# Performance work log

Measured on AMD Instinct MI355X. Metric: run time of the kernel, lower is better.

The kernel has to match this reference:

```python
import jax, jax.numpy as jnp
import numpy as np

EPS = 1e-8  # torch F.cosine_similarity eps


def _cosine_logits(emb, mem):
    # emb: [N, C], mem: [S, C] -> [N, S]
    num = emb @ mem.T
    denom = jnp.linalg.norm(emb, axis=1, keepdims=True) * jnp.linalg.norm(mem, axis=1)[None, :]
    return num / jnp.maximum(denom, EPS)


def setup_inputs() -> dict:
    key = jax.random.key(0)
    k1, k2, k3, k4 = jax.random.split(key, 4)
    N, S, C = 8192, 4096, 256
    return {
        "face": jax.random.normal(k1, (N, C), dtype=jnp.float32),
        "speech": jax.random.normal(k2, (N, C), dtype=jnp.float32),
        # init.normal_(mean=0, std=0.5)
        "speech_value_memory": 0.5 * jax.random.normal(k3, (S, C), dtype=jnp.float32),
        "face_key_memory": 0.5 * jax.random.normal(k4, (S, C), dtype=jnp.float32),
    }


def reference(face, speech, speech_value_memory, face_key_memory):
    # speech_encoder runs under torch.no_grad() -> stop_gradient; encoders abstracted as identity.
    speech_emb = jax.lax.stop_gradient(speech)
    face_emb = face

    speech_logits = _cosine_logits(speech_emb, speech_value_memory)      # [N, S]
    speech_address_log = jax.nn.log_softmax(speech_logits, axis=1)
    speech_address = jax.nn.softmax(speech_logits, axis=1)
    speech_emb_recall = speech_address @ speech_value_memory             # [N, C]

    face_logits = _cosine_logits(face_emb, face_key_memory)             # [N, S]
    face_address_log = jax.nn.log_softmax(face_logits, axis=1)
    face_address = jax.nn.softmax(face_logits, axis=1)
    face_emb_recall = face_address @ speech_value_memory                 # [N, C]

    return (speech_emb, speech_emb_recall, face_emb, face_emb_recall,
            speech_address_log, face_address_log)
```

## Files before the change

kernel.cpp:

```cpp
#include <hip/hip_runtime.h>
#include <hip/hip_bf16.h>
#include <cstdint>
#include <cstddef>

typedef __attribute__((ext_vector_type(8))) short bf16x8;
typedef __attribute__((ext_vector_type(4))) float f32x4;

static __device__ __forceinline__ unsigned short f2bf(float f) {
    union { float f; unsigned u; } v; v.f = f;
    return (unsigned short)((v.u + 0x7fffu + ((v.u >> 16) & 1u)) >> 16);
}
static __device__ __forceinline__ float bf2f(unsigned short h) {
    union { unsigned u; float f; } v; v.u = ((unsigned)h) << 16;
    return v.f;
}

static __device__ __forceinline__ void gld_lds16(const unsigned short* g, unsigned short* l) {
    __builtin_amdgcn_global_load_lds(
        (const __attribute__((address_space(1))) void*)g,
        (__attribute__((address_space(3))) void*)l, 16, 0, 0);
}

#define NC 2097152
#define SC 1048576
#define NS 33554432
#define SPLITS 4

__global__ __launch_bounds__(256) void rownorm_kernel(
    const float* __restrict__ face, const float* __restrict__ speech,
    const float* __restrict__ svm, const float* __restrict__ fkm,
    unsigned short* __restrict__ face_n, unsigned short* __restrict__ speech_n,
    unsigned short* __restrict__ svm_n, unsigned short* __restrict__ fkm_n,
    float* __restrict__ out_face, float* __restrict__ out_speech,
    unsigned short* __restrict__ svmT,
    float* __restrict__ out_srecall, float* __restrict__ out_frecall,
    float* __restrict__ sumexp)
{
    const int which = blockIdx.y;
    const int sub   = threadIdx.x >> 6;
    const int lane  = threadIdx.x & 63;
    const int row   = blockIdx.x * 4 + sub;

    if (which == 4) {
        const float4 z = make_float4(0.f, 0.f, 0.f, 0.f);
        *(float4*)(out_srecall + (size_t)row * 256 + lane * 4) = z;
        *(float4*)(out_frecall + (size_t)row * 256 + lane * 4) = z;
        if (lane < 2) sumexp[(size_t)lane * 8192 + row] = 0.f;
        return;
    }
    if (which >= 2 && row >= 4096) return;

    const float* in; unsigned short* nrm; float* cpy = nullptr; bool tr = false;
    if (which == 0)      { in = speech; nrm = speech_n; cpy = out_speech; }
    else if (which == 1) { in = face;   nrm = face_n;   cpy = out_face; }
    else if (which == 2) { in = svm;    nrm = svm_n;    tr = true; }
    else                 { in = fkm;    nrm = fkm_n; }

    const float4 v = *(const float4*)(in + (size_t)row * 256 + lane * 4);
    float ss = v.x * v.x + v.y * v.y + v.z * v.z + v.w * v.w;
    #pragma unroll
    for (int off = 32; off > 0; off >>= 1) ss += __shfl_xor(ss, off);
    const float rn = rsqrtf(ss);

    ushort4 o;
    o.x = f2bf(v.x * rn); o.y = f2bf(v.y * rn);
    o.z = f2bf(v.z * rn); o.w = f2bf(v.w * rn);
    *(ushort4*)(nrm + (size_t)row * 256 + lane * 4) = o;

    if (cpy) *(float4*)(cpy + (size_t)row * 256 + lane * 4) = v;

    if (tr) {
        const int c = lane * 4;
        svmT[(size_t)(c + 0) * 4096 + row] = f2bf(v.x);
        svmT[(size_t)(c + 1) * 4096 + row] = f2bf(v.y);
        svmT[(size_t)(c + 2) * 4096 + row] = f2bf(v.z);
        svmT[(size_t)(c + 3) * 4096 + row] = f2bf(v.w);
    }
}

__global__ __launch_bounds__(256) void gemm_logits_kernel(
    const unsigned short* __restrict__ speech_n,
    const unsigned short* __restrict__ face_n,
    const unsigned short* __restrict__ svm_n,
    const unsigned short* __restrict__ fkm_n,
    unsigned short* __restrict__ logits,
    float* __restrict__ sumexp)
{
    __shared__ unsigned short smem[128 * 32 * 2];
    unsigned short* As = smem;
    unsigned short* Bs = smem + 128 * 32;
    const int side = blockIdx.z;
    const unsigned short* A = side ? face_n : speech_n;
    const unsigned short* B = side ? fkm_n  : svm_n;
    unsigned short* Lg = logits + ((size_t)side * NS);

    const int row0 = blockIdx.y * 128;
    const int col0 = blockIdx.x * 128;
    const int tid  = threadIdx.x;
    const int wave = tid >> 6, lane = tid & 63;
    const int wm = (wave >> 1) * 64, wn = (wave & 1) * 64;
    const int quad = lane >> 4, r16 = lane & 15;

    const int r0 = tid >> 2,          cj0 = tid & 3;
    const int r1 = (tid + 256) >> 2,  cj1 = (tid + 256) & 3;

    f32x4 acc[4][4];
    #pragma unroll
    for (int i = 0; i < 4; i++)
        #pragma unroll
        for (int j = 0; j < 4; j++) acc[i][j] = 0.f;

    for (int k0 = 0; k0 < 256; k0 += 32) {
        gld_lds16(A + (size_t)(row0 + r0) * 256 + k0 + cj0 * 8, As + (size_t)(wave * 64) * 8);
        gld_lds16(B + (size_t)(col0 + r0) * 256 + k0 + cj0 * 8, Bs + (size_t)(wave * 64) * 8);
        gld_lds16(A + (size_t)(row0 + r1) * 256 + k0 + cj1 * 8, As + (size_t)(256 + wave * 64) * 8);
        gld_lds16(B + (size_t)(col0 + r1) * 256 + k0 + cj1 * 8, Bs + (size_t)(256 + wave * 64) * 8);
        __syncthreads();

        bf16x8 af[4], bfr[4];
        #pragma unroll
        for (int i = 0; i < 4; i++) {
            af[i]  = *(const bf16x8*)(&As[(wm + i * 16 + r16) * 32 + quad * 8]);
            bfr[i] = *(const bf16x8*)(&Bs[(wn + i * 16 + r16) * 32 + quad * 8]);
        }
        #pragma unroll
        for (int i = 0; i < 4; i++)
            #pragma unroll
            for (int j = 0; j < 4; j++)
                acc[i][j] = __builtin_amdgcn_mfma_f32_16x16x32_bf16(
                    af[i], bfr[j], acc[i][j], 0, 0, 0);
        __syncthreads();
    }

    #pragma unroll
    for (int i = 0; i < 4; i++) {
        #pragma unroll
        for (int rr = 0; rr < 4; rr++) {
            float s = 0.f;
            #pragma unroll
            for (int j = 0; j < 4; j++) s += __expf(acc[i][j][rr]);
            #pragma unroll
            for (int o = 8; o > 0; o >>= 1) s += __shfl_xor(s, o);
            if (r16 == 0)
                unsafeAtomicAdd(&sumexp[(size_t)side * 8192 + row0 + wm + i * 16 + quad * 4 + rr], s);
        }
    }

    unsigned short* tb = smem + wave * 2048;
    #pragma unroll
    for (int h = 0; h < 2; ++h) {
        #pragma unroll
        for (int i2 = 0; i2 < 2; ++i2)
            #pragma unroll
            for (int j = 0; j < 4; ++j)
                #pragma unroll
                for (int rr = 0; rr < 4; ++rr)
                    tb[(i2 * 16 + quad * 4 + rr) * 64 + j * 16 + r16] =
                        f2bf(acc[2 * h + i2][j][rr]);
        #pragma unroll
        for (int p = 0; p < 4; ++p) {
            const int lrow = p * 8 + (lane >> 3);
            const int lcol = (lane & 7) * 8;
            const uint4 v = *(const uint4*)(tb + lrow * 64 + lcol);
            *(uint4*)(Lg + (size_t)(row0 + wm + h * 32 + lrow) * 4096 + col0 + wn + lcol) = v;
        }
    }
}

__global__ __launch_bounds__(256) void gemm_recall_kernel(
    const unsigned short* __restrict__ logits,
    const float* __restrict__ sumexp,
    const unsigned short* __restrict__ BT,
    float* __restrict__ out_srecall, float* __restrict__ out_frecall,
    float* __restrict__ out_slog, float* __restrict__ out_flog)
{
    __shared__ unsigned short As[64 * 32];
    __shared__ unsigned short Bs[256 * 32];
    const int row0  = blockIdx.x * 64;
    const int split = blockIdx.y;
    const int side  = blockIdx.z;
    const unsigned short* A = logits + (size_t)side * NS;
    float* outp = side ? out_frecall : out_srecall;
    float* slog = side ? out_flog    : out_slog;
    const int kbase = split * (4096 / SPLITS);

    const int tid  = threadIdx.x;
    const int wave = tid >> 6, lane = tid & 63;
    const int wn = wave * 64;
    const int quad = lane >> 4, r16 = lane & 15;
    const int arow = tid >> 2, acj = tid & 3;
    const float myl = __logf(sumexp[(size_t)side * 8192 + row0 + arow]);
    float* slogp = slog + (size_t)(row0 + arow) * 4096 + acj * 8;

    f32x4 acc[4][4];
    #pragma unroll
    for (int i = 0; i < 4; i++)
        #pragma unroll
        for (int j = 0; j < 4; j++) acc[i][j] = 0.f;

    for (int k0 = kbase; k0 < kbase + 4096 / SPLITS; k0 += 32) {
        unsigned short vv[8];
        *(uint4*)vv = *(const uint4*)(A + (size_t)(row0 + arow) * 4096 + k0 + acj * 8);
        #pragma unroll
        for (int it = 0; it < 4; ++it) {
            const int c = tid + it * 256, r = c >> 2, cj = c & 3;
            gld_lds16(BT + (size_t)r * 4096 + k0 + cj * 8,
                      Bs + (size_t)(it * 256 + wave * 64) * 8);
        }
        float xs[8];
        #pragma unroll
        for (int k = 0; k < 8; k++) xs[k] = bf2f(vv[k]) - myl;
        f32x4 s0, s1;
        s0[0] = xs[0]; s0[1] = xs[1]; s0[2] = xs[2]; s0[3] = xs[3];
        s1[0] = xs[4]; s1[1] = xs[5]; s1[2] = xs[6]; s1[3] = xs[7];
        __builtin_nontemporal_store(s0, (f32x4*)(slogp + k0));
        __builtin_nontemporal_store(s1, (f32x4*)(slogp + k0 + 4));
        unsigned short pv[8];
        #pragma unroll
        for (int k = 0; k < 8; k++) pv[k] = f2bf(__expf(xs[k]));
        *(uint4*)(&As[arow * 32 + acj * 8]) = *(uint4*)pv;
        __syncthreads();

        bf16x8 af[4], bfr[4];
        #pragma unroll
        for (int i = 0; i < 4; i++) {
            af[i]  = *(const bf16x8*)(&As[(i * 16 + r16) * 32 + quad * 8]);
            bfr[i] = *(const bf16x8*)(&Bs[(wn + i * 16 + r16) * 32 + quad * 8]);
        }
        #pragma unroll
        for (int i = 0; i < 4; i++)
            #pragma unroll
            for (int j = 0; j < 4; j++)
                acc[i][j] = __builtin_amdgcn_mfma_f32_16x16x32_bf16(
                    af[i], bfr[j], acc[i][j], 0, 0, 0);
        __syncthreads();
    }

    #pragma unroll
    for (int i = 0; i < 4; i++) {
        #pragma unroll
        for (int j = 0; j < 4; j++) {
            const int r  = row0 + i * 16 + quad * 4;
            const int cc = wn + j * 16 + r16;
            #pragma unroll
            for (int rr = 0; rr < 4; rr++)
                unsafeAtomicAdd(&outp[(size_t)(r + rr) * 256 + cc], acc[i][j][rr]);
        }
    }
}

extern "C" void kernel_launch(void* const* d_in, const int* in_sizes, int n_in,
                              void* d_out, int out_size, void* d_ws, size_t ws_size,
                              hipStream_t stream) {
    const float* face   = (const float*)d_in[0];
    const float* speech = (const float*)d_in[1];
    const float* svm    = (const float*)d_in[2];
    const float* fkm    = (const float*)d_in[3];

    const int N = 8192, S = 4096, C = 256;
    float* out = (float*)d_out;
    float* out_speech  = out;
    float* out_srecall = out + (size_t)N * C;
    float* out_face    = out + 2 * (size_t)N * C;
    float* out_frecall = out + 3 * (size_t)N * C;
    float* out_slog    = out + 4 * (size_t)N * C;
    float* out_flog    = out_slog + (size_t)N * S;

    unsigned short* wsu = (unsigned short*)d_ws;
    unsigned short* speech_n = wsu;
    unsigned short* face_n   = speech_n + NC;
    unsigned short* svm_n    = face_n + NC;
    unsigned short* fkm_n    = svm_n + SC;
    unsigned short* svmT     = fkm_n + SC;
    unsigned short* logits   = svmT + SC;
    float* sumexp = (float*)(logits + 2 * (size_t)NS);

    dim3 g1(N / 4, 5);
    rownorm_kernel<<<g1, 256, 0, stream>>>(face, speech, svm, fkm,
                                           face_n, speech_n, svm_n, fkm_n,
                                           out_face, out_speech, svmT,
                                           out_srecall, out_frecall, sumexp);

    dim3 g2(S / 128, N / 128, 2);
    gemm_logits_kernel<<<g2, 256, 0, stream>>>(speech_n, face_n, svm_n, fkm_n,
                                               logits, sumexp);

    dim3 g4(N / 64, SPLITS, 2);
    gemm_recall_kernel<<<g4, 256, 0, stream>>>(logits, sumexp, svmT,
                                               out_srecall, out_frecall,
                                               out_slog, out_flog);
}
```

Before: 467.9 us.

## Double-buffer LDS tiles and prefetch logits in recall GEMM main loop

Adds double-buffered LDS for the A (softmax probabilities) and B (value memory) tiles in the recall GEMM. The next tile's global-to-LDS loads, logit register prefetch, exp conversion and log-softmax stores are issued before the current tile's MFMAs, and one barrier per iteration is removed. The aim is to hide global load latency behind matrix compute. In exchange it doubles LDS use per block, which may lower occupancy, and it raises register pressure from the extra prefetched vector.

```diff
diff --git a/kernel.cpp b/kernel.cpp
--- a/kernel.cpp
+++ b/kernel.cpp
@@ -174,8 +174,8 @@
     float* __restrict__ out_srecall, float* __restrict__ out_frecall,
     float* __restrict__ out_slog, float* __restrict__ out_flog)
 {
-    __shared__ unsigned short As[64 * 32];
-    __shared__ unsigned short Bs[256 * 32];
+    __shared__ unsigned short As[2][64 * 32];
+    __shared__ unsigned short Bs[2][256 * 32];
     const int row0  = blockIdx.x * 64;
     const int split = blockIdx.y;
     const int side  = blockIdx.z;
@@ -183,6 +183,7 @@
     float* outp = side ? out_frecall : out_srecall;
     float* slog = side ? out_flog    : out_slog;
     const int kbase = split * (4096 / SPLITS);
+    const int NT    = (4096 / SPLITS) / 32;
 
     const int tid  = threadIdx.x;
     const int wave = tid >> 6, lane = tid & 63;
@@ -190,6 +191,7 @@
     const int quad = lane >> 4, r16 = lane & 15;
     const int arow = tid >> 2, acj = tid & 3;
     const float myl = __logf(sumexp[(size_t)side * 8192 + row0 + arow]);
+    const unsigned short* Ar = A + (size_t)(row0 + arow) * 4096 + acj * 8;
     float* slogp = slog + (size_t)(row0 + arow) * 4096 + acj * 8;
 
     f32x4 acc[4][4];
@@ -198,34 +200,68 @@
         #pragma unroll
         for (int j = 0; j < 4; j++) acc[i][j] = 0.f;
 
-    for (int k0 = kbase; k0 < kbase + 4096 / SPLITS; k0 += 32) {
-        unsigned short vv[8];
-        *(uint4*)vv = *(const uint4*)(A + (size_t)(row0 + arow) * 4096 + k0 + acj * 8);
-        #pragma unroll
-        for (int it = 0; it < 4; ++it) {
-            const int c = tid + it * 256, r = c >> 2, cj = c & 3;
-            gld_lds16(BT + (size_t)r * 4096 + k0 + cj * 8,
-                      Bs + (size_t)(it * 256 + wave * 64) * 8);
-        }
+
+    uint4 a_cur  = *(const uint4*)(Ar + kbase);
+    #pragma unroll
+    for (int it = 0; it < 4; ++it) {
+        const int c = tid + it * 256, r = c >> 2, cj = c & 3;
+        gld_lds16(BT + (size_t)r * 4096 + kbase + cj * 8,
+                  &Bs[0][(size_t)(it * 256 + wave * 64) * 8]);
+    }
+    uint4 a_pend = *(const uint4*)(Ar + kbase + 32);
+    {
+        const unsigned short* vv = (const unsigned short*)&a_cur;
         float xs[8];
-        #pragma unroll
-        for (int k = 0; k < 8; k++) xs[k] = bf2f(vv[k]) - myl;
+        unsigned short pv[8];
+        #pragma unroll
+        for (int k = 0; k < 8; k++) {
+            xs[k] = bf2f(vv[k]) - myl;
+            pv[k] = f2bf(__expf(xs[k]));
+        }
+        *(uint4*)(&As[0][arow * 32 + acj * 8]) = *(uint4*)pv;
         f32x4 s0, s1;
-        s0[0] = xs[0]; s0[1] = xs[1]; s0[2] = xs[2]; s0[3] = xs[3];
-        s1[0] = xs[4]; s1[1] = xs[5]; s1[2] = xs[6]; s1[3] = xs[7];
-        __builtin_nontemporal_store(s0, (f32x4*)(slogp + k0));
-        __builtin_nontemporal_store(s1, (f32x4*)(slogp + k0 + 4));
-        unsigned short pv[8];
-        #pragma unroll
-        for (int k = 0; k < 8; k++) pv[k] = f2bf(__expf(xs[k]));
-        *(uint4*)(&As[arow * 32 + acj * 8]) = *(uint4*)pv;
-        __syncthreads();
+        #pragma unroll
+        for (int k = 0; k < 4; k++) { s0[k] = xs[k]; s1[k] = xs[k + 4]; }
+        __builtin_nontemporal_store(s0, (f32x4*)(slogp + kbase));
+        __builtin_nontemporal_store(s1, (f32x4*)(slogp + kbase + 4));
+    }
+    __syncthreads();
+
+    for (int t = 0; t < NT; ++t) {
+        const int c = t & 1, n = c ^ 1;
+
+        if (t + 1 < NT) {
+            const int k1 = kbase + (t + 1) * 32;
+            #pragma unroll
+            for (int it = 0; it < 4; ++it) {
+                const int cc = tid + it * 256, r = cc >> 2, cj = cc & 3;
+                gld_lds16(BT + (size_t)r * 4096 + k1 + cj * 8,
+                          &Bs[n][(size_t)(it * 256 + wave * 64) * 8]);
+            }
+            a_cur = a_pend;
+            if (t + 2 < NT)
+                a_pend = *(const uint4*)(Ar + kbase + (t + 2) * 32);
+            const unsigned short* vv = (const unsigned short*)&a_cur;
+            float xs[8];
+            unsigned short pv[8];
+            #pragma unroll
+            for (int k = 0; k < 8; k++) {
+                xs[k] = bf2f(vv[k]) - myl;
+                pv[k] = f2bf(__expf(xs[k]));
+            }
+            *(uint4*)(&As[n][arow * 32 + acj * 8]) = *(uint4*)pv;
+            f32x4 s0, s1;
+            #pragma unroll
+            for (int k = 0; k < 4; k++) { s0[k] = xs[k]; s1[k] = xs[k + 4]; }
+            __builtin_nontemporal_store(s0, (f32x4*)(slogp + k1));
+            __builtin_nontemporal_store(s1, (f32x4*)(slogp + k1 + 4));
+        }
 
         bf16x8 af[4], bfr[4];
         #pragma unroll
         for (int i = 0; i < 4; i++) {
-            af[i]  = *(const bf16x8*)(&As[(i * 16 + r16) * 32 + quad * 8]);
-            bfr[i] = *(const bf16x8*)(&Bs[(wn + i * 16 + r16) * 32 + quad * 8]);
+            af[i]  = *(const bf16x8*)(&As[c][(i * 16 + r16) * 32 + quad * 8]);
+            bfr[i] = *(const bf16x8*)(&Bs[c][(wn + i * 16 + r16) * 32 + quad * 8]);
         }
         #pragma unroll
         for (int i = 0; i < 4; i++)
@@ -233,6 +269,7 @@
             for (int j = 0; j < 4; j++)
                 acc[i][j] = __builtin_amdgcn_mfma_f32_16x16x32_bf16(
                     af[i], bfr[j], acc[i][j], 0, 0, 0);
+
         __syncthreads();
     }
 
```

Result: no change. 475.6 us (+1.6%).
